# Performance work log

Measured on AMD Instinct MI355X. Metric: run time of the kernel, lower is better.

The kernel has to match this reference:

```python
import jax, jax.numpy as jnp
import numpy as np

B, S, D, H = 2, 2048, 1024, 16
MAX_DIST = 1024


def setup_inputs() -> dict:
    key = jax.random.key(0)
    ks = jax.random.split(key, 7)
    w = lambda k, shape: jax.random.normal(k, shape, jnp.float32) * 0.02
    return {
        "x": jax.random.normal(ks[0], (B, S, D), jnp.float32),
        "Wq": w(ks[1], (D, D)), "bq": jnp.zeros((D,), jnp.float32),
        "Wk": w(ks[2], (D, D)),
        "Wv": w(ks[3], (D, D)), "bv": jnp.zeros((D,), jnp.float32),
        "Wo": w(ks[4], (D, D)), "bo": jnp.zeros((D,), jnp.float32),
        "pos_bias": w(ks[5], (2 * MAX_DIST - 1, H)),
        "max_dist": MAX_DIST,
    }


def reference(x, Wq, bq, Wk, Wv, bv, Wo, bo, pos_bias, max_dist):
    b, s, d_model = x.shape
    h = pos_bias.shape[1]
    hd = d_model // h  # head dim
    scale = hd ** -0.25  # module's scale applied to (QK^T + rel_bias)

    split = lambda t: t.reshape(b, s, h, hd).transpose(0, 2, 1, 3)  # [b,h,s,hd]
    q = split(x @ Wq + bq)
    k = split(x @ Wk)          # key has no bias
    v = split(x @ Wv + bv)

    # raw QK^T (unscaled), as in the module
    scores = jnp.einsum('bhqd,bhkd->bhqk', q, k)

    # relative-position bias gather: clamp(i-j) -> table index
    pos = jnp.arange(s)[:, None] - jnp.arange(s)[None, :]
    pos = jnp.clip(pos, -max_dist + 1, max_dist - 1) + max_dist - 1
    rel_bias = pos_bias[pos].transpose(2, 0, 1)[None]  # [1,h,s,s]

    # SDPA with attn_mask = (scores + rel_bias)*scale adds it on top of QK^T/sqrt(hd)
    logits = scores * (1.0 / jnp.sqrt(jnp.float32(hd))) + (scores + rel_bias) * scale
    w = jax.nn.softmax(logits, axis=-1)

    out = jnp.einsum('bhqk,bhkd->bhqd', w, v)
    out = out.transpose(0, 2, 1, 3).reshape(b, s, d_model)
    return out @ Wo + bo
```

## Files before the change

kernel.cpp:

```cpp
#include <hip/hip_runtime.h>
#include <hip/hip_bf16.h>
#include <cstddef>
#include <cstdint>

#define BATCH   2
#define S_LEN   2048
#define D_MODEL 1024
#define NH      16
#define HD      64
#define MAXD    1024

#define SCORE_SCALE 0.47855339059327373f
#define BIAS_SCALE  0.35355339059327373f
#define FIXM 8.0f
#define LOG2E 1.4426950408889634f

typedef __attribute__((ext_vector_type(8))) short bf16x8;
typedef __attribute__((ext_vector_type(4))) short bf16x4;
typedef __attribute__((ext_vector_type(4))) float f32x4;

#if __has_builtin(__builtin_amdgcn_mfma_f32_16x16x16bf16_1k)
#define USE_1K 1
#else
#define USE_1K 0
#endif

static __device__ __forceinline__ unsigned short f2bf(float f) {
    __hip_bfloat16 h = __float2bfloat16(f);
    return *reinterpret_cast<unsigned short*>(&h);
}
static __device__ __forceinline__ float bf2f(unsigned short u) {
    union { unsigned int i; float f; } c;
    c.i = ((unsigned int)u) << 16;
    return c.f;
}

#define GLDS(gp, lp) __builtin_amdgcn_global_load_lds( \
    (const __attribute__((address_space(1))) void*)(gp), \
    (__attribute__((address_space(3))) void*)(lp), 16, 0, 0)

__global__ __launch_bounds__(256) void prep(
    const float* __restrict__ x,
    const float* __restrict__ Wq, const float* __restrict__ Wk,
    const float* __restrict__ Wv, const float* __restrict__ Wo,
    const float* __restrict__ pos_bias,
    unsigned short* __restrict__ xb, unsigned short* __restrict__ Wqkvt,
    unsigned short* __restrict__ Wot_hi, unsigned short* __restrict__ Wot_lo,
    float* __restrict__ pb_t)
{
    __shared__ float t[32][33];
    const int bx = blockIdx.x, tid = threadIdx.x;

    if (bx < 2048) {
        const size_t i = ((size_t)bx * 256 + tid) * 8;
        const float4 a = *(const float4*)(x + i);
        const float4 b = *(const float4*)(x + i + 4);
        unsigned short u[8] = {f2bf(a.x), f2bf(a.y), f2bf(a.z), f2bf(a.w),
                               f2bf(b.x), f2bf(b.y), f2bf(b.z), f2bf(b.w)};
        *(uint4*)(xb + i) = *(const uint4*)u;
    } else if (bx < 6144) {
        const int bx2 = bx - 2048;
        const int z = bx2 >> 10, inner = bx2 & 1023;
        const int gx = inner & 31, gy = inner >> 5;
        const float* W = (z == 0) ? Wq : (z == 1) ? Wk : (z == 2) ? Wv : Wo;
        unsigned short* hi = (z < 3) ? Wqkvt + (size_t)z * 1024 * 1024 : Wot_hi;
        unsigned short* lo = (z == 3) ? Wot_lo : nullptr;
        const int bxx = gx * 32, byy = gy * 32;
        const int tx = tid & 31, ty = tid >> 5;
        #pragma unroll
        for (int i = 0; i < 4; i++)
            t[ty + 8 * i][tx] = W[(size_t)(byy + ty + 8 * i) * 1024 + bxx + tx];
        __syncthreads();
        #pragma unroll
        for (int i = 0; i < 4; i++) {
            const float v = t[tx][ty + 8 * i];
            const unsigned short hh = f2bf(v);
            const size_t o = (size_t)(bxx + ty + 8 * i) * 1024 + byy + tx;
            hi[o] = hh;
            if (lo) lo[o] = f2bf(v - bf2f(hh));
        }
    } else {
        const int o0 = (bx - 6144) * 1024 + tid * 4;
        float v[4];
        #pragma unroll
        for (int j = 0; j < 4; j++) {
            const int o = o0 + j;
            const int hh = o >> 12, ii = o & 4095;
            int rel = ii - 2047;
            rel = min(max(rel, -(MAXD - 1)), MAXD - 1);
            v[j] = (BIAS_SCALE * pos_bias[(size_t)(rel + MAXD - 1) * NH + hh] - FIXM) * LOG2E;
        }
        *(float4*)&pb_t[o0] = *(const float4*)v;
    }
}

#define GBM 128
#define GBN 128
#define GBK 32

__global__ __launch_bounds__(256) void gemm_qkv(
    const unsigned short* __restrict__ A, const unsigned short* __restrict__ Bt,
    const float* __restrict__ bq, const float* __restrict__ bv,
    unsigned short* __restrict__ Cout)
{
    const int K = 1024;
    __shared__ __align__(16) unsigned short As[GBM][GBK];
    __shared__ __align__(16) unsigned short Bs[GBN][GBK];

    const int tid = threadIdx.x;
    const int wave = tid >> 6, lane = tid & 63;
    const int quad = lane >> 4, cl = lane & 15;
    const int wm = (wave & 1) * 64, wn = (wave >> 1) * 64;
    const int bm = blockIdx.y * GBM, bn = blockIdx.x * GBN;

    const int sr = wave * 32 + (lane >> 2);
    const int sc = (lane & 3) * 8;
    const unsigned short* aS0 = A  + (size_t)(bm + sr) * K + sc;
    const unsigned short* aS1 = aS0 + (size_t)16 * K;
    const unsigned short* bS0 = Bt + (size_t)(bn + sr) * K + sc;
    const unsigned short* bS1 = bS0 + (size_t)16 * K;
    unsigned short* aD0 = &As[wave * 32][0];
    unsigned short* aD1 = &As[wave * 32 + 16][0];
    unsigned short* bD0 = &Bs[wave * 32][0];
    unsigned short* bD1 = &Bs[wave * 32 + 16][0];

    f32x4 acc[4][4];
    #pragma unroll
    for (int mi = 0; mi < 4; mi++)
        #pragma unroll
        for (int ni = 0; ni < 4; ni++)
            #pragma unroll
            for (int r = 0; r < 4; r++) acc[mi][ni][r] = 0.f;

    for (int k0 = 0; k0 < K; k0 += GBK) {
        __syncthreads();
        GLDS(aS0, aD0); GLDS(aS1, aD1);
        GLDS(bS0, bD0); GLDS(bS1, bD1);
        aS0 += GBK; aS1 += GBK; bS0 += GBK; bS1 += GBK;
        __syncthreads();

        bf16x8 af[4], bf[4];
        #pragma unroll
        for (int mi = 0; mi < 4; mi++)
            af[mi] = *(const bf16x8*)&As[wm + mi * 16 + cl][quad * 8];
        #pragma unroll
        for (int ni = 0; ni < 4; ni++)
            bf[ni] = *(const bf16x8*)&Bs[wn + ni * 16 + cl][quad * 8];
        #pragma unroll
        for (int mi = 0; mi < 4; mi++)
            #pragma unroll
            for (int ni = 0; ni < 4; ni++)
                acc[mi][ni] = __builtin_amdgcn_mfma_f32_16x16x32_bf16(
                    af[mi], bf[ni], acc[mi][ni], 0, 0, 0);
    }

    #pragma unroll
    for (int ni = 0; ni < 4; ni++) {
        const int coln = bn + wn + ni * 16 + cl;
        const int region = coln >> 10, c = coln & 1023;
        const float bs = (region == 0) ? bq[c] : (region == 2) ? bv[c] : 0.f;
        #pragma unroll
        for (int mi = 0; mi < 4; mi++) {
            const int row0 = bm + wm + mi * 16 + quad * 4;
            if (region == 2) {
                const int hh = c >> 6, d = c & 63;
                const int bb = row0 >> 11, s0 = row0 & 2047;
                unsigned short u[4];
                #pragma unroll
                for (int r = 0; r < 4; r++) u[r] = f2bf(acc[mi][ni][r] + bs);
                unsigned short* dst = Cout + (size_t)8 * 1024 * 1024
                    + (((size_t)bb * NH + hh) * HD + d) * S_LEN + s0;
                *(uint2*)dst = *(const uint2*)u;
            } else {
                unsigned short* dst = Cout + (size_t)region * 4 * 1024 * 1024;
                #pragma unroll
                for (int r = 0; r < 4; r++)
                    dst[(size_t)(row0 + r) * 1024 + c] = f2bf(acc[mi][ni][r] + bs);
            }
        }
    }
}

#define TQB 64
#define TKB 64

__global__ __launch_bounds__(256) void attn_mfma(
    const unsigned short* __restrict__ Q, const unsigned short* __restrict__ K,
    const unsigned short* __restrict__ VT, const float* __restrict__ pb_t,
    unsigned short* __restrict__ O)
{
    const int qt = blockIdx.x, h = blockIdx.y, b = blockIdx.z;
    const int tid  = threadIdx.x;
    const int wave = tid >> 6, lane = tid & 63;
    const int quad = lane >> 4, col = lane & 15;
    const int qbase = qt * TQB;
    const int qw = qbase + wave * 16;

    __shared__ __align__(16) unsigned short Ks[2][TKB][HD];
    __shared__ __align__(16) unsigned short Vs[2][HD][TKB];
#if !USE_1K
    __shared__ __align__(16) unsigned short Ps[4][16][TKB];
#endif

    bf16x8 qf[2];
    {
        const unsigned short* qp =
            &Q[((size_t)(b * S_LEN) + qw + col) * D_MODEL + h * HD + quad * 8];
        qf[0] = *(const bf16x8*)qp;
        qf[1] = *(const bf16x8*)(qp + 32);
    }

    f32x4 accO[4];
    #pragma unroll
    for (int nb = 0; nb < 4; nb++)
        #pragma unroll
        for (int r = 0; r < 4; r++) accO[nb][r] = 0.f;
#if USE_1K
    f32x4 accL;
    #pragma unroll
    for (int r = 0; r < 4; r++) accL[r] = 0.f;
    const bf16x4 vone = {(short)16256, (short)16256, (short)16256, (short)16256};
#else
    float lsum = 0.f;
#endif

    const int s0 = tid, s1 = 256 + tid;
    const int kr0 = s0 >> 3, kj0 = (s0 & 7) ^ (kr0 & 7);
    const int kr1 = s1 >> 3, kj1 = (s1 & 7) ^ (kr1 & 7);
    const unsigned short* kS0 = K + ((size_t)(b * S_LEN) + kr0) * D_MODEL + h * HD + kj0 * 8;
    const unsigned short* kS1 = K + ((size_t)(b * S_LEN) + kr1) * D_MODEL + h * HD + kj1 * 8;
    const size_t vbase = ((size_t)(b * NH + h) * HD) * S_LEN;
    const unsigned short* vS0 = VT + vbase + (size_t)kr0 * S_LEN + kj0 * 8;
    const unsigned short* vS1 = VT + vbase + (size_t)kr1 * S_LEN + kj1 * 8;

    {
        unsigned short* kb0 = &Ks[0][0][0] + wave * 512;
        unsigned short* vb0 = &Vs[0][0][0] + wave * 512;
        GLDS(kS0, kb0); GLDS(kS1, kb0 + 2048);
        GLDS(vS0, vb0); GLDS(vS1, vb0 + 2048);
        kS0 += (size_t)TKB * D_MODEL; kS1 += (size_t)TKB * D_MODEL;
        vS0 += TKB; vS1 += TKB;
    }
    __syncthreads();

    const float* pbh = pb_t + h * 4096;
    const float* pb_lane = pbh + (qbase + wave * 16 + col - quad * 4 + 2047);
    const float SC2 = SCORE_SCALE * LOG2E;
    const int jsw = col & 7;

    for (int kb = 0, t = 0; kb < S_LEN; kb += TKB, t++) {
        const int p = t & 1;
        if (kb + TKB < S_LEN) {
            unsigned short* kd = &Ks[p ^ 1][0][0] + wave * 512;
            unsigned short* vd = &Vs[p ^ 1][0][0] + wave * 512;
            GLDS(kS0, kd); GLDS(kS1, kd + 2048);
            GLDS(vS0, vd); GLDS(vS1, vd + 2048);
            kS0 += (size_t)TKB * D_MODEL; kS1 += (size_t)TKB * D_MODEL;
            vS0 += TKB; vS1 += TKB;
        }

        float bias_r[16];
        #pragma unroll
        for (int nb = 0; nb < 4; nb++)
            #pragma unroll
            for (int r = 0; r < 4; r++)
                bias_r[nb * 4 + r] = pb_lane[-(nb * 16 + r)];

        f32x4 accS[4];
        #pragma unroll
        for (int nb = 0; nb < 4; nb++)
            #pragma unroll
            for (int r = 0; r < 4; r++) accS[nb][r] = 0.f;
        #pragma unroll
        for (int kk = 0; kk < 2; kk++)
            #pragma unroll
            for (int nb = 0; nb < 4; nb++) {
                const bf16x8 kf = *(const bf16x8*)
                    &Ks[p][nb * 16 + col][((kk * 4 + quad) ^ jsw) * 8];
                accS[nb] = __builtin_amdgcn_mfma_f32_16x16x32_bf16(kf, qf[kk], accS[nb], 0, 0, 0);
            }

#if USE_1K
        bf16x4 pf[4];
#endif
        #pragma unroll
        for (int nb = 0; nb < 4; nb++) {
            float pr[4];
            #pragma unroll
            for (int r = 0; r < 4; r++)
                pr[r] = __builtin_amdgcn_exp2f(fmaf(accS[nb][r], SC2, bias_r[nb * 4 + r]));
            const __hip_bfloat162 h0 = __float22bfloat162_rn(make_float2(pr[0], pr[1]));
            const __hip_bfloat162 h1 = __float22bfloat162_rn(make_float2(pr[2], pr[3]));
            uint2 w;
            w.x = *(const unsigned int*)&h0;
            w.y = *(const unsigned int*)&h1;
#if USE_1K
            union { uint2 u; bf16x4 v; } cv;
            cv.u = w;
            pf[nb] = cv.v;
            accL = __builtin_amdgcn_mfma_f32_16x16x16bf16_1k(vone, pf[nb], accL, 0, 0, 0);
#else
            #pragma unroll
            for (int r = 0; r < 4; r++) lsum += pr[r];
            const int jp = ((nb * 2 + (quad >> 1)) ^ jsw) * 8 + (quad & 1) * 4;
            *(uint2*)&Ps[wave][col][jp] = w;
#endif
        }

#if USE_1K
        #pragma unroll
        for (int s = 0; s < 4; s++) {
            #pragma unroll
            for (int nb = 0; nb < 4; nb++) {
                const bf16x4 vf = *(const bf16x4*)
                    &Vs[p][nb * 16 + col][(((2 * s + (quad >> 1)) ^ jsw) * 8) + (quad & 1) * 4];
                accO[nb] = __builtin_amdgcn_mfma_f32_16x16x16bf16_1k(vf, pf[s], accO[nb], 0, 0, 0);
            }
        }
#else
        #pragma unroll
        for (int kk = 0; kk < 2; kk++) {
            const bf16x8 af = *(const bf16x8*)
                &Ps[wave][col][((kk * 4 + quad) ^ jsw) * 8];
            #pragma unroll
            for (int nb = 0; nb < 4; nb++) {
                const bf16x8 vf = *(const bf16x8*)
                    &Vs[p][nb * 16 + col][((kk * 4 + quad) ^ jsw) * 8];
                accO[nb] = __builtin_amdgcn_mfma_f32_16x16x32_bf16(af, vf, accO[nb], 0, 0, 0);
            }
        }
#endif
        pb_lane -= TKB;
        __syncthreads();
    }

#if USE_1K
    const float inv = 1.0f / accL[0];
    const size_t row = (size_t)(b * S_LEN) + qw + col;
    #pragma unroll
    for (int nb = 0; nb < 4; nb++) {
        unsigned short u[4];
        #pragma unroll
        for (int r = 0; r < 4; r++) u[r] = f2bf(accO[nb][r] * inv);
        *(uint2*)&O[row * D_MODEL + h * HD + nb * 16 + quad * 4] = *(const uint2*)u;
    }
#else
    lsum += __shfl_xor(lsum, 16);
    lsum += __shfl_xor(lsum, 32);
    #pragma unroll
    for (int r = 0; r < 4; r++) {
        const float inv = 1.0f / __shfl(lsum, quad * 4 + r);
        const size_t row = (size_t)(b * S_LEN) + qw + quad * 4 + r;
        #pragma unroll
        for (int nb = 0; nb < 4; nb++)
            O[row * D_MODEL + h * HD + nb * 16 + col] = f2bf(accO[nb][r] * inv);
    }
#endif
}

#define OBM 64
#define OBN 128

__global__ __launch_bounds__(256) void gemm_out(
    const unsigned short* __restrict__ A, const unsigned short* __restrict__ Bhi,
    const unsigned short* __restrict__ Blo, const float* __restrict__ bias,
    float* __restrict__ Cout)
{
    const int N = 1024, Kd = 1024;
    __shared__ __align__(16) unsigned short As[OBM][GBK];
    __shared__ __align__(16) unsigned short Bs[2][OBN][GBK];

    const int tid = threadIdx.x;
    const int wave = tid >> 6, lane = tid & 63;
    const int quad = lane >> 4, cl = lane & 15;
    const int wm = (wave & 1) * 32, wn = (wave >> 1) * 64;
    const int bm = blockIdx.y * OBM, bn = blockIdx.x * OBN;

    const int ar = tid >> 2, ac = (tid & 3) * 8;
    const unsigned short* aS = A + (size_t)(bm + ar) * Kd + ac;
    const unsigned short* hS0 = Bhi + (size_t)(bn + ar) * Kd + ac;
    const unsigned short* hS1 = hS0 + (size_t)64 * Kd;
    const unsigned short* lS0 = Blo + (size_t)(bn + ar) * Kd + ac;
    const unsigned short* lS1 = lS0 + (size_t)64 * Kd;
    unsigned short* aD  = &As[0][0] + wave * 512;
    unsigned short* hD0 = &Bs[0][0][0] + wave * 512;
    unsigned short* hD1 = hD0 + 2048;
    unsigned short* lD0 = &Bs[1][0][0] + wave * 512;
    unsigned short* lD1 = lD0 + 2048;

    f32x4 acc[2][4];
    #pragma unroll
    for (int mi = 0; mi < 2; mi++)
        #pragma unroll
        for (int ni = 0; ni < 4; ni++)
            #pragma unroll
            for (int r = 0; r < 4; r++) acc[mi][ni][r] = 0.f;

    for (int k0 = 0; k0 < Kd; k0 += GBK) {
        __syncthreads();
        GLDS(aS, aD);
        GLDS(hS0, hD0); GLDS(hS1, hD1);
        GLDS(lS0, lD0); GLDS(lS1, lD1);
        aS += GBK; hS0 += GBK; hS1 += GBK; lS0 += GBK; lS1 += GBK;
        __syncthreads();

        bf16x8 af[2], bh[4];
        #pragma unroll
        for (int mi = 0; mi < 2; mi++)
            af[mi] = *(const bf16x8*)&As[wm + mi * 16 + cl][quad * 8];
        #pragma unroll
        for (int ni = 0; ni < 4; ni++)
            bh[ni] = *(const bf16x8*)&Bs[0][wn + ni * 16 + cl][quad * 8];
        #pragma unroll
        for (int mi = 0; mi < 2; mi++)
            #pragma unroll
            for (int ni = 0; ni < 4; ni++)
                acc[mi][ni] = __builtin_amdgcn_mfma_f32_16x16x32_bf16(
                    af[mi], bh[ni], acc[mi][ni], 0, 0, 0);
        #pragma unroll
        for (int ni = 0; ni < 4; ni++)
            bh[ni] = *(const bf16x8*)&Bs[1][wn + ni * 16 + cl][quad * 8];
        #pragma unroll
        for (int mi = 0; mi < 2; mi++)
            #pragma unroll
            for (int ni = 0; ni < 4; ni++)
                acc[mi][ni] = __builtin_amdgcn_mfma_f32_16x16x32_bf16(
                    af[mi], bh[ni], acc[mi][ni], 0, 0, 0);
    }

    #pragma unroll
    for (int ni = 0; ni < 4; ni++) {
        const int coln = bn + wn + ni * 16 + cl;
        const float bs = bias[coln];
        #pragma unroll
        for (int mi = 0; mi < 2; mi++) {
            const int row0 = bm + wm + mi * 16 + quad * 4;
            #pragma unroll
            for (int r = 0; r < 4; r++)
                Cout[(size_t)(row0 + r) * N + coln] = acc[mi][ni][r] + bs;
        }
    }
}

extern "C" void kernel_launch(void* const* d_in, const int* in_sizes, int n_in,
                              void* d_out, int out_size, void* d_ws, size_t ws_size,
                              hipStream_t stream)
{
    const float* x        = (const float*)d_in[0];
    const float* Wq       = (const float*)d_in[1];
    const float* bq       = (const float*)d_in[2];
    const float* Wk       = (const float*)d_in[3];
    const float* Wv       = (const float*)d_in[4];
    const float* bv       = (const float*)d_in[5];
    const float* Wo       = (const float*)d_in[6];
    const float* bo       = (const float*)d_in[7];
    const float* pos_bias = (const float*)d_in[8];
    float* out = (float*)d_out;

    const size_t ELEMS  = (size_t)BATCH * S_LEN * D_MODEL;
    const size_t WELEMS = (size_t)D_MODEL * D_MODEL;
    unsigned short* xb     = (unsigned short*)d_ws;
    unsigned short* Wqkvt  = xb + ELEMS;
    unsigned short* Wot_hi = Wqkvt + 3 * WELEMS;
    unsigned short* Wot_lo = Wot_hi + WELEMS;
    unsigned short* QKV    = Wot_lo + WELEMS;
    unsigned short* Qb     = QKV;
    unsigned short* Kb     = Qb + ELEMS;
    unsigned short* VTb    = Kb + ELEMS;
    unsigned short* Ab     = VTb + ELEMS;
    float* pb_t            = (float*)(Ab + ELEMS);

    prep<<<6208, 256, 0, stream>>>(x, Wq, Wk, Wv, Wo, pos_bias,
                                   xb, Wqkvt, Wot_hi, Wot_lo, pb_t);

    gemm_qkv<<<dim3(3072 / GBN, 4096 / GBM), 256, 0, stream>>>(
        xb, Wqkvt, bq, bv, QKV);

    attn_mfma<<<dim3(S_LEN / TQB, NH, BATCH), 256, 0, stream>>>(
        Qb, Kb, VTb, pb_t, Ab);

    gemm_out<<<dim3(1024 / OBN, 4096 / OBM), 256, 0, stream>>>(
        Ab, Wot_hi, Wot_lo, bo, out);
}
```

Before: 222.1 us.

## Drop hi/lo split of Wo and single-buffer attention K/V tiles

```diff
diff --git a/kernel.cpp b/kernel.cpp
--- a/kernel.cpp
+++ b/kernel.cpp
@@ -45,7 +45,7 @@
     const float* __restrict__ Wv, const float* __restrict__ Wo,
     const float* __restrict__ pos_bias,
     unsigned short* __restrict__ xb, unsigned short* __restrict__ Wqkvt,
-    unsigned short* __restrict__ Wot_hi, unsigned short* __restrict__ Wot_lo,
+    unsigned short* __restrict__ Wot,
     float* __restrict__ pb_t)
 {
     __shared__ float t[32][33];
@@ -63,8 +63,7 @@
         const int z = bx2 >> 10, inner = bx2 & 1023;
         const int gx = inner & 31, gy = inner >> 5;
         const float* W = (z == 0) ? Wq : (z == 1) ? Wk : (z == 2) ? Wv : Wo;
-        unsigned short* hi = (z < 3) ? Wqkvt + (size_t)z * 1024 * 1024 : Wot_hi;
-        unsigned short* lo = (z == 3) ? Wot_lo : nullptr;
+        unsigned short* hi = (z < 3) ? Wqkvt + (size_t)z * 1024 * 1024 : Wot;
         const int bxx = gx * 32, byy = gy * 32;
         const int tx = tid & 31, ty = tid >> 5;
         #pragma unroll
@@ -74,10 +73,8 @@
         #pragma unroll
         for (int i = 0; i < 4; i++) {
             const float v = t[tx][ty + 8 * i];
-            const unsigned short hh = f2bf(v);
             const size_t o = (size_t)(bxx + ty + 8 * i) * 1024 + byy + tx;
-            hi[o] = hh;
-            if (lo) lo[o] = f2bf(v - bf2f(hh));
+            hi[o] = f2bf(v);
         }
     } else {
         const int o0 = (bx - 6144) * 1024 + tid * 4;
@@ -196,8 +193,8 @@
     const int qbase = qt * TQB;
     const int qw = qbase + wave * 16;
 
-    __shared__ __align__(16) unsigned short Ks[2][TKB][HD];
-    __shared__ __align__(16) unsigned short Vs[2][HD][TKB];
+    __shared__ __align__(16) unsigned short Ks[TKB][HD];
+    __shared__ __align__(16) unsigned short Vs[HD][TKB];
 #if !USE_1K
     __shared__ __align__(16) unsigned short Ps[4][16][TKB];
 #endif
@@ -232,32 +229,20 @@
     const size_t vbase = ((size_t)(b * NH + h) * HD) * S_LEN;
     const unsigned short* vS0 = VT + vbase + (size_t)kr0 * S_LEN + kj0 * 8;
     const unsigned short* vS1 = VT + vbase + (size_t)kr1 * S_LEN + kj1 * 8;
-
-    {
-        unsigned short* kb0 = &Ks[0][0][0] + wave * 512;
-        unsigned short* vb0 = &Vs[0][0][0] + wave * 512;
-        GLDS(kS0, kb0); GLDS(kS1, kb0 + 2048);
-        GLDS(vS0, vb0); GLDS(vS1, vb0 + 2048);
-        kS0 += (size_t)TKB * D_MODEL; kS1 += (size_t)TKB * D_MODEL;
-        vS0 += TKB; vS1 += TKB;
-    }
-    __syncthreads();
+    unsigned short* kD = &Ks[0][0] + wave * 512;
+    unsigned short* vD = &Vs[0][0] + wave * 512;
 
     const float* pbh = pb_t + h * 4096;
     const float* pb_lane = pbh + (qbase + wave * 16 + col - quad * 4 + 2047);
     const float SC2 = SCORE_SCALE * LOG2E;
     const int jsw = col & 7;
 
-    for (int kb = 0, t = 0; kb < S_LEN; kb += TKB, t++) {
-        const int p = t & 1;
-        if (kb + TKB < S_LEN) {
-            unsigned short* kd = &Ks[p ^ 1][0][0] + wave * 512;
-            unsigned short* vd = &Vs[p ^ 1][0][0] + wave * 512;
-            GLDS(kS0, kd); GLDS(kS1, kd + 2048);
-            GLDS(vS0, vd); GLDS(vS1, vd + 2048);
-            kS0 += (size_t)TKB * D_MODEL; kS1 += (size_t)TKB * D_MODEL;
-            vS0 += TKB; vS1 += TKB;
-        }
+    for (int kb = 0; kb < S_LEN; kb += TKB) {
+        __syncthreads();
+        GLDS(kS0, kD); GLDS(kS1, kD + 2048);
+        GLDS(vS0, vD); GLDS(vS1, vD + 2048);
+        kS0 += (size_t)TKB * D_MODEL; kS1 += (size_t)TKB * D_MODEL;
+        vS0 += TKB; vS1 += TKB;
 
         float bias_r[16];
         #pragma unroll
@@ -266,6 +251,8 @@
             for (int r = 0; r < 4; r++)
                 bias_r[nb * 4 + r] = pb_lane[-(nb * 16 + r)];
 
+        __syncthreads();
+
         f32x4 accS[4];
         #pragma unroll
         for (int nb = 0; nb < 4; nb++)
@@ -276,7 +263,7 @@
             #pragma unroll
             for (int nb = 0; nb < 4; nb++) {
                 const bf16x8 kf = *(const bf16x8*)
-                    &Ks[p][nb * 16 + col][((kk * 4 + quad) ^ jsw) * 8];
+                    &Ks[nb * 16 + col][((kk * 4 + quad) ^ jsw) * 8];
                 accS[nb] = __builtin_amdgcn_mfma_f32_16x16x32_bf16(kf, qf[kk], accS[nb], 0, 0, 0);
             }
 
@@ -313,7 +300,7 @@
             #pragma unroll
             for (int nb = 0; nb < 4; nb++) {
                 const bf16x4 vf = *(const bf16x4*)
-                    &Vs[p][nb * 16 + col][(((2 * s + (quad >> 1)) ^ jsw) * 8) + (quad & 1) * 4];
+                    &Vs[nb * 16 + col][(((2 * s + (quad >> 1)) ^ jsw) * 8) + (quad & 1) * 4];
                 accO[nb] = __builtin_amdgcn_mfma_f32_16x16x16bf16_1k(vf, pf[s], accO[nb], 0, 0, 0);
             }
         }
@@ -325,13 +312,12 @@
             #pragma unroll
             for (int nb = 0; nb < 4; nb++) {
                 const bf16x8 vf = *(const bf16x8*)
-                    &Vs[p][nb * 16 + col][((kk * 4 + quad) ^ jsw) * 8];
+                    &Vs[nb * 16 + col][((kk * 4 + quad) ^ jsw) * 8];
                 accO[nb] = __builtin_amdgcn_mfma_f32_16x16x32_bf16(af, vf, accO[nb], 0, 0, 0);
             }
         }
 #endif
         pb_lane -= TKB;
-        __syncthreads();
     }
 
 #if USE_1K
@@ -362,13 +348,12 @@
 #define OBN 128
 
 __global__ __launch_bounds__(256) void gemm_out(
-    const unsigned short* __restrict__ A, const unsigned short* __restrict__ Bhi,
-    const unsigned short* __restrict__ Blo, const float* __restrict__ bias,
-    float* __restrict__ Cout)
+    const unsigned short* __restrict__ A, const unsigned short* __restrict__ Bt,
+    const float* __restrict__ bias, float* __restrict__ Cout)
 {
     const int N = 1024, Kd = 1024;
     __shared__ __align__(16) unsigned short As[OBM][GBK];
-    __shared__ __align__(16) unsigned short Bs[2][OBN][GBK];
+    __shared__ __align__(16) unsigned short Bs[OBN][GBK];
 
     const int tid = threadIdx.x;
     const int wave = tid >> 6, lane = tid & 63;
@@ -378,15 +363,11 @@
 
     const int ar = tid >> 2, ac = (tid & 3) * 8;
     const unsigned short* aS = A + (size_t)(bm + ar) * Kd + ac;
-    const unsigned short* hS0 = Bhi + (size_t)(bn + ar) * Kd + ac;
+    const unsigned short* hS0 = Bt + (size_t)(bn + ar) * Kd + ac;
     const unsigned short* hS1 = hS0 + (size_t)64 * Kd;
-    const unsigned short* lS0 = Blo + (size_t)(bn + ar) * Kd + ac;
-    const unsigned short* lS1 = lS0 + (size_t)64 * Kd;
     unsigned short* aD  = &As[0][0] + wave * 512;
-    unsigned short* hD0 = &Bs[0][0][0] + wave * 512;
+    unsigned short* hD0 = &Bs[0][0] + wave * 512;
     unsigned short* hD1 = hD0 + 2048;
-    unsigned short* lD0 = &Bs[1][0][0] + wave * 512;
-    unsigned short* lD1 = lD0 + 2048;
 
     f32x4 acc[2][4];
     #pragma unroll
@@ -400,8 +381,7 @@
         __syncthreads();
         GLDS(aS, aD);
         GLDS(hS0, hD0); GLDS(hS1, hD1);
-        GLDS(lS0, lD0); GLDS(lS1, lD1);
-        aS += GBK; hS0 += GBK; hS1 += GBK; lS0 += GBK; lS1 += GBK;
+        aS += GBK; hS0 += GBK; hS1 += GBK;
         __syncthreads();
 
         bf16x8 af[2], bh[4];
@@ -410,16 +390,7 @@
             af[mi] = *(const bf16x8*)&As[wm + mi * 16 + cl][quad * 8];
         #pragma unroll
         for (int ni = 0; ni < 4; ni++)
-            bh[ni] = *(const bf16x8*)&Bs[0][wn + ni * 16 + cl][quad * 8];
-        #pragma unroll
-        for (int mi = 0; mi < 2; mi++)
-            #pragma unroll
-            for (int ni = 0; ni < 4; ni++)
-                acc[mi][ni] = __builtin_amdgcn_mfma_f32_16x16x32_bf16(
-                    af[mi], bh[ni], acc[mi][ni], 0, 0, 0);
-        #pragma unroll
-        for (int ni = 0; ni < 4; ni++)
-            bh[ni] = *(const bf16x8*)&Bs[1][wn + ni * 16 + cl][quad * 8];
+            bh[ni] = *(const bf16x8*)&Bs[wn + ni * 16 + cl][quad * 8];
         #pragma unroll
         for (int mi = 0; mi < 2; mi++)
             #pragma unroll
@@ -461,9 +432,8 @@
     const size_t WELEMS = (size_t)D_MODEL * D_MODEL;
     unsigned short* xb     = (unsigned short*)d_ws;
     unsigned short* Wqkvt  = xb + ELEMS;
-    unsigned short* Wot_hi = Wqkvt + 3 * WELEMS;
-    unsigned short* Wot_lo = Wot_hi + WELEMS;
-    unsigned short* QKV    = Wot_lo + WELEMS;
+    unsigned short* Wot    = Wqkvt + 3 * WELEMS;
+    unsigned short* QKV    = Wot + WELEMS;
     unsigned short* Qb     = QKV;
     unsigned short* Kb     = Qb + ELEMS;
     unsigned short* VTb    = Kb + ELEMS;
@@ -471,7 +441,7 @@
     float* pb_t            = (float*)(Ab + ELEMS);
 
     prep<<<6208, 256, 0, stream>>>(x, Wq, Wk, Wv, Wo, pos_bias,
-                                   xb, Wqkvt, Wot_hi, Wot_lo, pb_t);
+                                   xb, Wqkvt, Wot, pb_t);
 
     gemm_qkv<<<dim3(3072 / GBN, 4096 / GBM), 256, 0, stream>>>(
         xb, Wqkvt, bq, bv, QKV);
@@ -480,5 +450,5 @@
         Qb, Kb, VTb, pb_t, Ab);
 
     gemm_out<<<dim3(1024 / OBN, 4096 / OBM), 256, 0, stream>>>(
-        Ab, Wot_hi, Wot_lo, bo, out);
-}
+        Ab, Wot, bo, out);
+}
```

Result: faster. 206.1 us (-7.2%).
